# Kernel optimization log

Measured on AMD Instinct MI355X. Metric: run time of the kernel, lower is better.

## Reference

```python
import jax, jax.numpy as jnp
import numpy as np

HEADS = 16
GROUPS = 4
C_IN = 1024
C_OUT = 1024


def att_linear(x, w, b):
    # x: [B,S,C_in], w: [G, C_in/G, C_out/G], b: [C_out]
    B, S, _ = x.shape
    xg = x.reshape(B, S, GROUPS, C_IN // GROUPS)
    out = jnp.einsum('bsgi,gio->bsgo', xg, w).reshape(B, S, C_OUT)
    return out + b


def restricted_softmax(score, margin=0.0):
    # clamp row max at 0, add exp(margin - max) margin term to denominator
    smax = jnp.maximum(jnp.max(score, axis=-1, keepdims=True), 0.0)
    e = jnp.exp(score - smax)
    return e / (jnp.sum(e, axis=-1, keepdims=True) + jnp.exp(margin - smax))


def setup_inputs() -> dict:
    key = jax.random.key(0)
    ks = jax.random.split(key, 9)
    B, S = 4, 1024
    dpg_in, dpg_out = C_IN // GROUPS, C_OUT // GROUPS
    wscale = 1.0 / np.sqrt(dpg_in)
    return {
        'query': jax.random.normal(ks[0], (B, S, C_IN), jnp.float32),
        'key': jax.random.normal(ks[1], (B, S, C_IN), jnp.float32),
        'value': jax.random.normal(ks[2], (B, S, C_IN), jnp.float32),
        'wq': jax.random.uniform(ks[3], (GROUPS, dpg_in, dpg_out), jnp.float32, -wscale, wscale),
        'bq': jax.random.uniform(ks[4], (C_OUT,), jnp.float32, -wscale, wscale),
        'wk': jax.random.uniform(ks[5], (GROUPS, dpg_in, dpg_out), jnp.float32, -wscale, wscale),
        'bk': jax.random.uniform(ks[6], (C_OUT,), jnp.float32, -wscale, wscale),
        'wv': jax.random.uniform(ks[7], (GROUPS, dpg_in, dpg_out), jnp.float32, -wscale, wscale),
        'bv': jax.random.uniform(ks[8], (C_OUT,), jnp.float32, -wscale, wscale),
    }


def reference(query, key, value, wq, bq, wk, bk, wv, bv):
    B, S, _ = query.shape
    d = C_OUT // HEADS
    q = att_linear(query, wq, bq).reshape(B, S, HEADS, d).transpose(0, 2, 1, 3)
    k = att_linear(key, wk, bk).reshape(B, S, HEADS, d).transpose(0, 2, 1, 3)
    v = att_linear(value, wv, bv).reshape(B, S, HEADS, d).transpose(0, 2, 1, 3)
    score = jnp.einsum('bhqd,bhkd->bhqk', q, k) / jnp.sqrt(jnp.float32(d))
    attn = restricted_softmax(score)  # dropout p=0
    out = jnp.einsum('bhqk,bhkd->bhqd', attn, v)
    return out.transpose(0, 2, 1, 3).reshape(B, S, C_OUT)
```

## Files before the change

### kernel.cpp

```cpp
#include <hip/hip_runtime.h>
#include <hip/hip_bf16.h>

#define HEADS   16
#define GROUPS  4
#define C_IN    1024
#define C_OUT   1024
#define BATCH   4
#define SEQ     1024
#define DHEAD   64
#define DPG     256
#define MROWS   (BATCH * SEQ)
#define NBH     (BATCH * HEADS)
#define W_ELEMS ((size_t)GROUPS * DPG * DPG)
#define N_ELEMS ((size_t)NBH * SEQ * DHEAD)

typedef short  bhalf8  __attribute__((ext_vector_type(8)));
typedef short  short4v __attribute__((ext_vector_type(4)));
typedef float  f32x4   __attribute__((ext_vector_type(4)));
typedef unsigned short ushort8v __attribute__((ext_vector_type(8)));

#define MFMA16 __builtin_amdgcn_mfma_f32_16x16x32_bf16

__device__ __forceinline__ unsigned short f2bf(float x) {
    union { __hip_bfloat16 b; unsigned short u; } c;
    c.b = __float2bfloat16(x);
    return c.u;
}
__device__ __forceinline__ float bf2f(unsigned short s) {
    return __uint_as_float(((unsigned int)s) << 16);
}

__global__ void wsplit(const float* __restrict__ w0,
                       const float* __restrict__ w1,
                       const float* __restrict__ w2,
                       unsigned short* __restrict__ wtbase)
{
    const int tid = threadIdx.x;
    const int kt = blockIdx.x, ot = blockIdx.y;
    const int which = blockIdx.z >> 2, g = blockIdx.z & 3;
    const float* w = (which == 0) ? w0 : (which == 1) ? w1 : w2;
    unsigned short* wth = wtbase + (size_t)which * 2 * W_ELEMS;
    unsigned short* wtl = wth + W_ELEMS;

    __shared__ float Ls[64][68];
    const float* wg = w + (size_t)g * DPG * DPG;
#pragma unroll
    for (int p = 0; p < 4; ++p) {
        const int kk = 16 * p + (tid >> 4);
        const int oo = 4 * (tid & 15);
        const float4 v = *reinterpret_cast<const float4*>(
            wg + (size_t)(kt * 64 + kk) * DPG + ot * 64 + oo);
        Ls[kk][oo + 0] = v.x; Ls[kk][oo + 1] = v.y;
        Ls[kk][oo + 2] = v.z; Ls[kk][oo + 3] = v.w;
    }
    __syncthreads();
    unsigned short* th = wth + (size_t)g * DPG * DPG;
    unsigned short* tl = wtl + (size_t)g * DPG * DPG;
#pragma unroll
    for (int p = 0; p < 4; ++p) {
        const int oo = 16 * p + (tid >> 4);
        const int k4 = 4 * (tid & 15);
        ushort4 hv, lv;
        {
            float v0 = Ls[k4 + 0][oo], v1 = Ls[k4 + 1][oo];
            float v2 = Ls[k4 + 2][oo], v3 = Ls[k4 + 3][oo];
            hv.x = f2bf(v0); lv.x = f2bf(v0 - bf2f(hv.x));
            hv.y = f2bf(v1); lv.y = f2bf(v1 - bf2f(hv.y));
            hv.z = f2bf(v2); lv.z = f2bf(v2 - bf2f(hv.z));
            hv.w = f2bf(v3); lv.w = f2bf(v3 - bf2f(hv.w));
        }
        const size_t o = (size_t)(ot * 64 + oo) * DPG + kt * 64 + k4;
        *reinterpret_cast<ushort4*>(th + o) = hv;
        *reinterpret_cast<ushort4*>(tl + o) = lv;
    }
}

__launch_bounds__(256, 2)
__global__ void proj_mfma(const float* __restrict__ xq,
                          const float* __restrict__ xk,
                          const float* __restrict__ xv,
                          const unsigned short* __restrict__ wtbase,
                          const float* __restrict__ bq,
                          const float* __restrict__ bk,
                          const float* __restrict__ bv,
                          unsigned short* __restrict__ outbase)
{
    const int tid  = threadIdx.x;
    const int wave = tid >> 6;
    const int lane = tid & 63;
    const int h    = lane >> 4;
    const int ln   = lane & 15;
    const int mq   = wave >> 1;
    const int nq   = wave & 1;
    const int bx   = blockIdx.x;
    const int by   = blockIdx.y;
    const int which = blockIdx.z >> 2, g = blockIdx.z & 3;
    const int m0   = bx * 64;

    const float* x    = (which == 0) ? xq : (which == 1) ? xk : xv;
    const float* bias = (which == 0) ? bq : (which == 1) ? bk : bv;
    unsigned short* outh = outbase + (size_t)which * 2 * N_ELEMS;
    unsigned short* outl = outh + N_ELEMS;

    __shared__ uint4 smem4[3072];
    char* sp = (char*)smem4;

    f32x4 acc[2][4];
#pragma unroll
    for (int a = 0; a < 2; ++a)
#pragma unroll
        for (int b = 0; b < 4; ++b) acc[a][b] = (f32x4){0.f, 0.f, 0.f, 0.f};

    const float* xg = x + (size_t)m0 * C_IN + g * DPG;
    const unsigned short* wh = wtbase + (size_t)which * 2 * W_ELEMS
                             + ((size_t)g * DPG + by * 128) * DPG;
    const unsigned short* wl = wh + W_ELEMS;

    const int arb = tid >> 4, ac = tid & 15;
    const int brb = tid >> 3, bc = tid & 7;

    float4   ar[4];
    ushort8v brh[4], brl[4];
#pragma unroll
    for (int p = 0; p < 4; ++p)
        ar[p] = *reinterpret_cast<const float4*>(xg + (size_t)(16 * p + arb) * C_IN + 4 * ac);
#pragma unroll
    for (int p = 0; p < 4; ++p) {
        const size_t gofs = (size_t)(32 * p + brb) * DPG + 8 * bc;
        brh[p] = *reinterpret_cast<const ushort8v*>(wh + gofs);
        brl[p] = *reinterpret_cast<const ushort8v*>(wl + gofs);
    }

    for (int it = 0; it < 4; ++it) {
        if (it > 0) __syncthreads();
#pragma unroll
        for (int p = 0; p < 4; ++p) {
            const int rr = 16 * p + arb;
            const float4 v = ar[p];
            ushort4 hv, lv;
            hv.x = f2bf(v.x); lv.x = f2bf(v.x - bf2f(hv.x));
            hv.y = f2bf(v.y); lv.y = f2bf(v.y - bf2f(hv.y));
            hv.z = f2bf(v.z); lv.z = f2bf(v.z - bf2f(hv.z));
            hv.w = f2bf(v.w); lv.w = f2bf(v.w - bf2f(hv.w));
            const int off = (8 * ac) ^ ((rr & 7) << 4);
            *reinterpret_cast<ushort4*>(sp + rr * 128 + off) = hv;
            *reinterpret_cast<ushort4*>(sp + 8192 + rr * 128 + off) = lv;
        }
#pragma unroll
        for (int p = 0; p < 4; ++p) {
            const int rr = 32 * p + brb;
            const int off = (16 * bc) ^ ((rr & 7) << 4);
            *reinterpret_cast<ushort8v*>(sp + 16384 + rr * 128 + off) = brh[p];
            *reinterpret_cast<ushort8v*>(sp + 32768 + rr * 128 + off) = brl[p];
        }
        __syncthreads();

        if (it < 3) {
            const int k0n = (it + 1) * 64;
#pragma unroll
            for (int p = 0; p < 4; ++p)
                ar[p] = *reinterpret_cast<const float4*>(
                    xg + (size_t)(16 * p + arb) * C_IN + k0n + 4 * ac);
#pragma unroll
            for (int p = 0; p < 4; ++p) {
                const size_t gofs = (size_t)(32 * p + brb) * DPG + k0n + 8 * bc;
                brh[p] = *reinterpret_cast<const ushort8v*>(wh + gofs);
                brl[p] = *reinterpret_cast<const ushort8v*>(wl + gofs);
            }
        }

#pragma unroll
        for (int kk = 0; kk < 2; ++kk) {
            bhalf8 ah[2], al[2], bh_[4], bl_[4];
#pragma unroll
            for (int mt = 0; mt < 2; ++mt) {
                const int row = 32 * mq + 16 * mt + ln;
                const int off = (64 * kk + 16 * h) ^ ((row & 7) << 4);
                ah[mt] = *reinterpret_cast<const bhalf8*>(sp + row * 128 + off);
                al[mt] = *reinterpret_cast<const bhalf8*>(sp + 8192 + row * 128 + off);
            }
#pragma unroll
            for (int nt = 0; nt < 4; ++nt) {
                const int row = 64 * nq + 16 * nt + ln;
                const int off = (64 * kk + 16 * h) ^ ((row & 7) << 4);
                bh_[nt] = *reinterpret_cast<const bhalf8*>(sp + 16384 + row * 128 + off);
                bl_[nt] = *reinterpret_cast<const bhalf8*>(sp + 32768 + row * 128 + off);
            }
#pragma unroll
            for (int mt = 0; mt < 2; ++mt)
#pragma unroll
                for (int nt = 0; nt < 4; ++nt) {
                    acc[mt][nt] = MFMA16(ah[mt], bh_[nt], acc[mt][nt], 0, 0, 0);
                    acc[mt][nt] = MFMA16(al[mt], bh_[nt], acc[mt][nt], 0, 0, 0);
                    acc[mt][nt] = MFMA16(ah[mt], bl_[nt], acc[mt][nt], 0, 0, 0);
                }
        }
    }
    __syncthreads();

    const int hd = g * 4 + by * 2 + nq;
    const int b  = bx >> 4;
    const size_t bhb = ((size_t)b * HEADS + hd) * (SEQ * DHEAD);
    const int wbase = wave * 8192;
    const int sg0 = (bx & 15) * 64 + 32 * mq;
    const float oscale = (which == 0) ? 0.125f : 1.0f;
    float bnt[4];
#pragma unroll
    for (int nt = 0; nt < 4; ++nt)
        bnt[nt] = bias[g * 256 + by * 128 + 64 * nq + 16 * nt + ln];

    if (which != 2) {
#pragma unroll
        for (int mt = 0; mt < 2; ++mt)
#pragma unroll
            for (int nt = 0; nt < 4; ++nt)
#pragma unroll
                for (int r = 0; r < 4; ++r) {
                    const int sl = 16 * mt + 4 * h + r;
                    const float v = (acc[mt][nt][r] + bnt[nt]) * oscale;
                    const unsigned short hh = f2bf(v);
                    const unsigned short ll = f2bf(v - bf2f(hh));
                    const int cb = (2 * (16 * nt + ln)) ^ ((sl & 7) << 4);
                    *reinterpret_cast<unsigned short*>(sp + wbase + sl * 128 + cb) = hh;
                    *reinterpret_cast<unsigned short*>(sp + wbase + 4096 + sl * 128 + cb) = ll;
                }
        __syncthreads();
#pragma unroll
        for (int p = 0; p < 4; ++p) {
            const int sl = 8 * p + (lane >> 3);
            const int cb = (16 * (lane & 7)) ^ ((sl & 7) << 4);
            const size_t go = bhb + (size_t)(sg0 + sl) * 64 + 8 * (lane & 7);
            *reinterpret_cast<ushort8v*>(outh + go) =
                *reinterpret_cast<const ushort8v*>(sp + wbase + sl * 128 + cb);
            *reinterpret_cast<ushort8v*>(outl + go) =
                *reinterpret_cast<const ushort8v*>(sp + wbase + 4096 + sl * 128 + cb);
        }
    } else {
#pragma unroll
        for (int mt = 0; mt < 2; ++mt)
#pragma unroll
            for (int nt = 0; nt < 4; ++nt) {
                const int dl = 16 * nt + ln;
                ushort4 hv, lv;
                {
                    float v0 = acc[mt][nt][0] + bnt[nt];
                    float v1 = acc[mt][nt][1] + bnt[nt];
                    float v2 = acc[mt][nt][2] + bnt[nt];
                    float v3 = acc[mt][nt][3] + bnt[nt];
                    hv.x = f2bf(v0); lv.x = f2bf(v0 - bf2f(hv.x));
                    hv.y = f2bf(v1); lv.y = f2bf(v1 - bf2f(hv.y));
                    hv.z = f2bf(v2); lv.z = f2bf(v2 - bf2f(hv.z));
                    hv.w = f2bf(v3); lv.w = f2bf(v3 - bf2f(hv.w));
                }
                const int off = (32 * mt + 8 * h) ^ ((dl & 7) << 3);
                *reinterpret_cast<ushort4*>(sp + wbase + dl * 64 + off) = hv;
                *reinterpret_cast<ushort4*>(sp + wbase + 4096 + dl * 64 + off) = lv;
            }
        __syncthreads();
#pragma unroll
        for (int p = 0; p < 4; ++p) {
            const int dl  = 16 * p + (lane >> 2);
            const int c16 = 16 * (lane & 3);
            const int o0b = (c16) ^ ((dl & 7) << 3);
            const int o1b = (c16 + 8) ^ ((dl & 7) << 3);
            const size_t go = bhb + (size_t)dl * SEQ + sg0 + 8 * (lane & 3);
            *reinterpret_cast<ushort4*>(outh + go) =
                *reinterpret_cast<const ushort4*>(sp + wbase + dl * 64 + o0b);
            *reinterpret_cast<ushort4*>(outh + go + 4) =
                *reinterpret_cast<const ushort4*>(sp + wbase + dl * 64 + o1b);
            *reinterpret_cast<ushort4*>(outl + go) =
                *reinterpret_cast<const ushort4*>(sp + wbase + 4096 + dl * 64 + o0b);
            *reinterpret_cast<ushort4*>(outl + go + 4) =
                *reinterpret_cast<const ushort4*>(sp + wbase + 4096 + dl * 64 + o1b);
        }
    }
}

__launch_bounds__(256, 2)
__global__ void attn_mfma(const unsigned short* __restrict__ qh,
                          const unsigned short* __restrict__ ql,
                          const unsigned short* __restrict__ kh,
                          const unsigned short* __restrict__ kl,
                          const unsigned short* __restrict__ vth,
                          const unsigned short* __restrict__ vtl,
                          float* __restrict__ out)
{
    const int tid  = threadIdx.x;
    const int wave = tid >> 6;
    const int lane = tid & 63;
    const int h    = lane >> 4;
    const int ln   = lane & 15;
    const int bh   = blockIdx.x;
    const int q0   = blockIdx.y * 128 + wave * 32;

    const size_t bhbase = (size_t)bh * (SEQ * DHEAD);
    const unsigned short* qhp = qh + bhbase;
    const unsigned short* qlp = ql + bhbase;
    const unsigned short* khp = kh + bhbase;
    const unsigned short* klp = kl + bhbase;
    const unsigned short* vhp = vth + bhbase;
    const unsigned short* vlp = vtl + bhbase;

    __shared__ uint4 smem4[2048];
    char* sb = (char*)smem4;

    bhalf8 Qf[2][2][2];
#pragma unroll
    for (int nt = 0; nt < 2; ++nt)
#pragma unroll
        for (int dt = 0; dt < 2; ++dt) {
            const size_t o = (size_t)(q0 + 16 * nt + ln) * DHEAD + dt * 32 + 8 * h;
            Qf[nt][dt][0] = *reinterpret_cast<const bhalf8*>(qhp + o);
            Qf[nt][dt][1] = *reinterpret_cast<const bhalf8*>(qlp + o);
        }

    f32x4 accO[2][4];
#pragma unroll
    for (int a = 0; a < 2; ++a)
#pragma unroll
        for (int b = 0; b < 4; ++b) accO[a][b] = (f32x4){0.f, 0.f, 0.f, 0.f};
    float m_i[2] = {0.f, 0.f};
    float l_i[2] = {1.f, 1.f};

    const int r = tid >> 2, c = tid & 3;
    const int swz = (r & 7) << 4;
    const int d0 = r * 128 + ((c * 32) ^ swz);
    const int d1 = r * 128 + ((c * 32 + 16) ^ swz);
    const size_t gKr = (size_t)r * DHEAD + c * 16;
    const size_t gVr = (size_t)r * SEQ + c * 16;

    uint4 pr[8];
    {
        pr[0] = *reinterpret_cast<const uint4*>(khp + gKr);
        pr[1] = *reinterpret_cast<const uint4*>(khp + gKr + 8);
        pr[2] = *reinterpret_cast<const uint4*>(klp + gKr);
        pr[3] = *reinterpret_cast<const uint4*>(klp + gKr + 8);
        pr[4] = *reinterpret_cast<const uint4*>(vhp + gVr);
        pr[5] = *reinterpret_cast<const uint4*>(vhp + gVr + 8);
        pr[6] = *reinterpret_cast<const uint4*>(vlp + gVr);
        pr[7] = *reinterpret_cast<const uint4*>(vlp + gVr + 8);
    }

    for (int kt16 = 0; kt16 < 16; ++kt16) {
        if (kt16 > 0) __syncthreads();
        *reinterpret_cast<uint4*>(sb + d0)         = pr[0];
        *reinterpret_cast<uint4*>(sb + d1)         = pr[1];
        *reinterpret_cast<uint4*>(sb + 8192 + d0)  = pr[2];
        *reinterpret_cast<uint4*>(sb + 8192 + d1)  = pr[3];
        *reinterpret_cast<uint4*>(sb + 16384 + d0) = pr[4];
        *reinterpret_cast<uint4*>(sb + 16384 + d1) = pr[5];
        *reinterpret_cast<uint4*>(sb + 24576 + d0) = pr[6];
        *reinterpret_cast<uint4*>(sb + 24576 + d1) = pr[7];
        __syncthreads();

        if (kt16 < 15) {
            const size_t gK = gKr + (size_t)(kt16 + 1) * 64 * DHEAD;
            const size_t gV = gVr + (size_t)(kt16 + 1) * 64;
            pr[0] = *reinterpret_cast<const uint4*>(khp + gK);
            pr[1] = *reinterpret_cast<const uint4*>(khp + gK + 8);
            pr[2] = *reinterpret_cast<const uint4*>(klp + gK);
            pr[3] = *reinterpret_cast<const uint4*>(klp + gK + 8);
            pr[4] = *reinterpret_cast<const uint4*>(vhp + gV);
            pr[5] = *reinterpret_cast<const uint4*>(vhp + gV + 8);
            pr[6] = *reinterpret_cast<const uint4*>(vlp + gV);
            pr[7] = *reinterpret_cast<const uint4*>(vlp + gV + 8);
        }

        f32x4 s_[2][4];
#pragma unroll
        for (int a = 0; a < 2; ++a)
#pragma unroll
            for (int b = 0; b < 4; ++b) s_[a][b] = (f32x4){0.f, 0.f, 0.f, 0.f};
#pragma unroll
        for (int mt = 0; mt < 4; ++mt) {
            const int rr = 16 * mt + ln;
            const int sw = (rr & 7) << 4;
            const bhalf8 Ah0 = *reinterpret_cast<const bhalf8*>(sb + rr * 128 + ((16 * h) ^ sw));
            const bhalf8 Ah1 = *reinterpret_cast<const bhalf8*>(sb + rr * 128 + ((64 + 16 * h) ^ sw));
            const bhalf8 Al0 = *reinterpret_cast<const bhalf8*>(sb + 8192 + rr * 128 + ((16 * h) ^ sw));
            const bhalf8 Al1 = *reinterpret_cast<const bhalf8*>(sb + 8192 + rr * 128 + ((64 + 16 * h) ^ sw));
#pragma unroll
            for (int nt = 0; nt < 2; ++nt) {
                s_[nt][mt] = MFMA16(Ah0, Qf[nt][0][0], s_[nt][mt], 0, 0, 0);
                s_[nt][mt] = MFMA16(Ah1, Qf[nt][1][0], s_[nt][mt], 0, 0, 0);
                s_[nt][mt] = MFMA16(Ah0, Qf[nt][0][1], s_[nt][mt], 0, 0, 0);
                s_[nt][mt] = MFMA16(Ah1, Qf[nt][1][1], s_[nt][mt], 0, 0, 0);
                s_[nt][mt] = MFMA16(Al0, Qf[nt][0][0], s_[nt][mt], 0, 0, 0);
                s_[nt][mt] = MFMA16(Al1, Qf[nt][1][0], s_[nt][mt], 0, 0, 0);
            }
        }

        float Pv[2][4][4];
        bhalf8 Pfh[2][2], Pfl[2][2];
#pragma unroll
        for (int nt = 0; nt < 2; ++nt) {
            float mloc = -1e30f;
#pragma unroll
            for (int mt = 0; mt < 4; ++mt)
#pragma unroll
                for (int rr = 0; rr < 4; ++rr) {
                    const float v = s_[nt][mt][rr];
                    Pv[nt][mt][rr] = v;
                    mloc = fmaxf(mloc, v);
                }
            mloc = fmaxf(mloc, __shfl_xor(mloc, 16));
            mloc = fmaxf(mloc, __shfl_xor(mloc, 32));
            const float mn = fmaxf(m_i[nt], mloc);
            const float sf = __expf(m_i[nt] - mn);
            m_i[nt] = mn;
            float rs = 0.f;
#pragma unroll
            for (int mt = 0; mt < 4; ++mt)
#pragma unroll
                for (int rr = 0; rr < 4; ++rr) {
                    const float p = __expf(Pv[nt][mt][rr] - mn);
                    Pv[nt][mt][rr] = p;
                    rs += p;
                }
            rs += __shfl_xor(rs, 16);
            rs += __shfl_xor(rs, 32);
            l_i[nt] = l_i[nt] * sf + rs;
#pragma unroll
            for (int rr = 0; rr < 4; ++rr) {
                const float sf_b = __shfl(sf, 20 * h + rr);
#pragma unroll
                for (int ntd = 0; ntd < 4; ++ntd) accO[nt][ntd][rr] *= sf_b;
            }
#pragma unroll
            for (int kt = 0; kt < 2; ++kt) {
                bhalf8 fh, fl;
#pragma unroll
                for (int j = 0; j < 8; ++j) {
                    const float p = Pv[nt][2 * kt + (j >> 2)][j & 3];
                    const unsigned short hi = f2bf(p);
                    fh[j] = (short)hi;
                    fl[j] = (short)f2bf(p - bf2f(hi));
                }
                Pfh[nt][kt] = fh;
                Pfl[nt][kt] = fl;
            }
        }

#pragma unroll
        for (int kt = 0; kt < 2; ++kt) {
#pragma unroll
            for (int ntd = 0; ntd < 4; ++ntd) {
                const int rr = 16 * ntd + ln;
                const int sw = (rr & 7) << 4;
                const int c0 = (64 * kt + 8 * h) ^ sw;
                const int c1 = (64 * kt + 32 + 8 * h) ^ sw;
                union { short4v q[2]; bhalf8 v; } ubh, ubl;
                ubh.q[0] = *reinterpret_cast<const short4v*>(sb + 16384 + rr * 128 + c0);
                ubh.q[1] = *reinterpret_cast<const short4v*>(sb + 16384 + rr * 128 + c1);
                ubl.q[0] = *reinterpret_cast<const short4v*>(sb + 24576 + rr * 128 + c0);
                ubl.q[1] = *reinterpret_cast<const short4v*>(sb + 24576 + rr * 128 + c1);
                const bhalf8 Bh = ubh.v;
                const bhalf8 Bl = ubl.v;
#pragma unroll
                for (int nt = 0; nt < 2; ++nt) {
                    accO[nt][ntd] = MFMA16(Pfh[nt][kt], Bh, accO[nt][ntd], 0, 0, 0);
                    accO[nt][ntd] = MFMA16(Pfh[nt][kt], Bl, accO[nt][ntd], 0, 0, 0);
                    accO[nt][ntd] = MFMA16(Pfl[nt][kt], Bh, accO[nt][ntd], 0, 0, 0);
                }
            }
        }
    }

    const int bB = bh >> 4;
    const int hd = bh & 15;
#pragma unroll
    for (int nt = 0; nt < 2; ++nt) {
        float linv[4];
#pragma unroll
        for (int rr = 0; rr < 4; ++rr) linv[rr] = 1.0f / __shfl(l_i[nt], 20 * h + rr);
#pragma unroll
        for (int rr = 0; rr < 4; ++rr) {
            const int q = q0 + 16 * nt + 4 * h + rr;
            float* orow = out + ((size_t)bB * SEQ + q) * C_OUT + hd * DHEAD + ln;
#pragma unroll
            for (int ntd = 0; ntd < 4; ++ntd)
                orow[16 * ntd] = accO[nt][ntd][rr] * linv[rr];
        }
    }
}

extern "C" void kernel_launch(void* const* d_in, const int* in_sizes, int n_in,
                              void* d_out, int out_size, void* d_ws, size_t ws_size,
                              hipStream_t stream) {
    const float* query = (const float*)d_in[0];
    const float* key   = (const float*)d_in[1];
    const float* value = (const float*)d_in[2];
    const float* wq    = (const float*)d_in[3];
    const float* bq    = (const float*)d_in[4];
    const float* wk    = (const float*)d_in[5];
    const float* bk    = (const float*)d_in[6];
    const float* wv    = (const float*)d_in[7];
    const float* bv    = (const float*)d_in[8];

    unsigned short* qkv = (unsigned short*)d_ws;
    unsigned short* wts = qkv + 6 * N_ELEMS;

    dim3 blk(256);
    wsplit<<<dim3(4, 4, 12), blk, 0, stream>>>(wq, wk, wv, wts);
    proj_mfma<<<dim3(MROWS / 64, 2, 12), blk, 0, stream>>>(
        query, key, value, wts, bq, bk, bv, qkv);

    attn_mfma<<<dim3(NBH, SEQ / 128), blk, 0, stream>>>(
        qkv, qkv + N_ELEMS, qkv + 2 * N_ELEMS, qkv + 3 * N_ELEMS,
        qkv + 4 * N_ELEMS, qkv + 5 * N_ELEMS, (float*)d_out);
}
```

Measured before the change: 224.5 us.

## Stage K/V and weight tiles via direct global-to-LDS loads with double buffering

```diff
diff --git a/kernel.cpp b/kernel.cpp
--- a/kernel.cpp
+++ b/kernel.cpp
@@ -28,6 +28,13 @@
 }
 __device__ __forceinline__ float bf2f(unsigned short s) {
     return __uint_as_float(((unsigned int)s) << 16);
+}
+
+__device__ __forceinline__ void gload16(const void* gsrc, void* lds) {
+    __builtin_amdgcn_global_load_lds(
+        (const __attribute__((address_space(1))) unsigned int*)(unsigned long long)(uintptr_t)gsrc,
+        (__attribute__((address_space(3))) unsigned int*)(unsigned int)(uintptr_t)lds,
+        16, 0, 0);
 }
 
 __global__ void wsplit(const float* __restrict__ w0,
@@ -116,27 +123,31 @@
                              + ((size_t)g * DPG + by * 128) * DPG;
     const unsigned short* wl = wh + W_ELEMS;
 
+    int b_goff[4], b_lds[4];
+#pragma unroll
+    for (int c = 0; c < 4; ++c) {
+        const int o  = (c * 4 + wave) * 1024 + lane * 16;
+        const int rw = o >> 7;
+        const int kidx = ((o & 127) ^ ((rw & 7) << 4)) >> 1;
+        b_goff[c] = rw * DPG + kidx;
+        b_lds[c]  = (c * 4 + wave) * 1024;
+    }
+
     const int arb = tid >> 4, ac = tid & 15;
-    const int brb = tid >> 3, bc = tid & 7;
-
-    float4   ar[4];
-    ushort8v brh[4], brl[4];
-#pragma unroll
-    for (int p = 0; p < 4; ++p)
-        ar[p] = *reinterpret_cast<const float4*>(xg + (size_t)(16 * p + arb) * C_IN + 4 * ac);
-#pragma unroll
-    for (int p = 0; p < 4; ++p) {
-        const size_t gofs = (size_t)(32 * p + brb) * DPG + 8 * bc;
-        brh[p] = *reinterpret_cast<const ushort8v*>(wh + gofs);
-        brl[p] = *reinterpret_cast<const ushort8v*>(wl + gofs);
-    }
 
     for (int it = 0; it < 4; ++it) {
+        const int k0 = it * 64;
         if (it > 0) __syncthreads();
+#pragma unroll
+        for (int c = 0; c < 4; ++c) {
+            gload16(wh + b_goff[c] + k0, sp + 16384 + b_lds[c]);
+            gload16(wl + b_goff[c] + k0, sp + 32768 + b_lds[c]);
+        }
 #pragma unroll
         for (int p = 0; p < 4; ++p) {
             const int rr = 16 * p + arb;
-            const float4 v = ar[p];
+            const float4 v = *reinterpret_cast<const float4*>(
+                xg + (size_t)rr * C_IN + k0 + 4 * ac);
             ushort4 hv, lv;
             hv.x = f2bf(v.x); lv.x = f2bf(v.x - bf2f(hv.x));
             hv.y = f2bf(v.y); lv.y = f2bf(v.y - bf2f(hv.y));
@@ -146,28 +157,7 @@
             *reinterpret_cast<ushort4*>(sp + rr * 128 + off) = hv;
             *reinterpret_cast<ushort4*>(sp + 8192 + rr * 128 + off) = lv;
         }
-#pragma unroll
-        for (int p = 0; p < 4; ++p) {
-            const int rr = 32 * p + brb;
-            const int off = (16 * bc) ^ ((rr & 7) << 4);
-            *reinterpret_cast<ushort8v*>(sp + 16384 + rr * 128 + off) = brh[p];
-            *reinterpret_cast<ushort8v*>(sp + 32768 + rr * 128 + off) = brl[p];
-        }
         __syncthreads();
-
-        if (it < 3) {
-            const int k0n = (it + 1) * 64;
-#pragma unroll
-            for (int p = 0; p < 4; ++p)
-                ar[p] = *reinterpret_cast<const float4*>(
-                    xg + (size_t)(16 * p + arb) * C_IN + k0n + 4 * ac);
-#pragma unroll
-            for (int p = 0; p < 4; ++p) {
-                const size_t gofs = (size_t)(32 * p + brb) * DPG + k0n + 8 * bc;
-                brh[p] = *reinterpret_cast<const ushort8v*>(wh + gofs);
-                brl[p] = *reinterpret_cast<const ushort8v*>(wl + gofs);
-            }
-        }
 
 #pragma unroll
         for (int kk = 0; kk < 2; ++kk) {
@@ -301,7 +291,7 @@
     const unsigned short* vhp = vth + bhbase;
     const unsigned short* vlp = vtl + bhbase;
 
-    __shared__ uint4 smem4[2048];
+    __shared__ uint4 smem4[4096];
     char* sb = (char*)smem4;
 
     bhalf8 Qf[2][2][2];
@@ -322,49 +312,37 @@
     float m_i[2] = {0.f, 0.f};
     float l_i[2] = {1.f, 1.f};
 
-    const int r = tid >> 2, c = tid & 3;
-    const int swz = (r & 7) << 4;
-    const int d0 = r * 128 + ((c * 32) ^ swz);
-    const int d1 = r * 128 + ((c * 32 + 16) ^ swz);
-    const size_t gKr = (size_t)r * DHEAD + c * 16;
-    const size_t gVr = (size_t)r * SEQ + c * 16;
-
-    uint4 pr[8];
-    {
-        pr[0] = *reinterpret_cast<const uint4*>(khp + gKr);
-        pr[1] = *reinterpret_cast<const uint4*>(khp + gKr + 8);
-        pr[2] = *reinterpret_cast<const uint4*>(klp + gKr);
-        pr[3] = *reinterpret_cast<const uint4*>(klp + gKr + 8);
-        pr[4] = *reinterpret_cast<const uint4*>(vhp + gVr);
-        pr[5] = *reinterpret_cast<const uint4*>(vhp + gVr + 8);
-        pr[6] = *reinterpret_cast<const uint4*>(vlp + gVr);
-        pr[7] = *reinterpret_cast<const uint4*>(vlp + gVr + 8);
-    }
-
-    for (int kt16 = 0; kt16 < 16; ++kt16) {
-        if (kt16 > 0) __syncthreads();
-        *reinterpret_cast<uint4*>(sb + d0)         = pr[0];
-        *reinterpret_cast<uint4*>(sb + d1)         = pr[1];
-        *reinterpret_cast<uint4*>(sb + 8192 + d0)  = pr[2];
-        *reinterpret_cast<uint4*>(sb + 8192 + d1)  = pr[3];
-        *reinterpret_cast<uint4*>(sb + 16384 + d0) = pr[4];
-        *reinterpret_cast<uint4*>(sb + 16384 + d1) = pr[5];
-        *reinterpret_cast<uint4*>(sb + 24576 + d0) = pr[6];
-        *reinterpret_cast<uint4*>(sb + 24576 + d1) = pr[7];
-        __syncthreads();
-
-        if (kt16 < 15) {
-            const size_t gK = gKr + (size_t)(kt16 + 1) * 64 * DHEAD;
-            const size_t gV = gVr + (size_t)(kt16 + 1) * 64;
-            pr[0] = *reinterpret_cast<const uint4*>(khp + gK);
-            pr[1] = *reinterpret_cast<const uint4*>(khp + gK + 8);
-            pr[2] = *reinterpret_cast<const uint4*>(klp + gK);
-            pr[3] = *reinterpret_cast<const uint4*>(klp + gK + 8);
-            pr[4] = *reinterpret_cast<const uint4*>(vhp + gV);
-            pr[5] = *reinterpret_cast<const uint4*>(vhp + gV + 8);
-            pr[6] = *reinterpret_cast<const uint4*>(vlp + gV);
-            pr[7] = *reinterpret_cast<const uint4*>(vlp + gV + 8);
-        }
+    int rw_[2], kd_[2], lofs_[2];
+#pragma unroll
+    for (int c = 0; c < 2; ++c) {
+        const int o = (c * 4 + wave) * 1024 + lane * 16;
+        rw_[c]   = o >> 7;
+        kd_[c]   = ((o & 127) ^ ((rw_[c] & 7) << 4)) >> 1;
+        lofs_[c] = (c * 4 + wave) * 1024;
+    }
+
+#define STAGE_TILE(BUF, K0)                                                        \
+    do {                                                                           \
+        _Pragma("unroll")                                                          \
+        for (int c = 0; c < 2; ++c) {                                              \
+            char* lb = sb + (BUF) + lofs_[c];                                      \
+            const int rw = rw_[c], kd = kd_[c];                                    \
+            gload16(khp + (size_t)((K0) + rw) * DHEAD + kd, lb);                   \
+            gload16(klp + (size_t)((K0) + rw) * DHEAD + kd, lb + 8192);            \
+            gload16(vhp + (size_t)rw * SEQ + (K0) + kd,     lb + 16384);           \
+            gload16(vlp + (size_t)rw * SEQ + (K0) + kd,     lb + 24576);           \
+        }                                                                          \
+    } while (0)
+
+    STAGE_TILE(0, 0);
+
+    for (int t = 0; t < 16; ++t) {
+        const int nb = ((t + 1) & 1) * 32768;
+        const int nk = ((t + 1) & 15) * 64;
+        STAGE_TILE(nb, nk);
+        asm volatile("s_waitcnt vmcnt(8)\n\ts_barrier" ::: "memory");
+
+        const char* cb = sb + (t & 1) * 32768;
 
         f32x4 s_[2][4];
 #pragma unroll
@@ -375,10 +353,10 @@
         for (int mt = 0; mt < 4; ++mt) {
             const int rr = 16 * mt + ln;
             const int sw = (rr & 7) << 4;
-            const bhalf8 Ah0 = *reinterpret_cast<const bhalf8*>(sb + rr * 128 + ((16 * h) ^ sw));
-            const bhalf8 Ah1 = *reinterpret_cast<const bhalf8*>(sb + rr * 128 + ((64 + 16 * h) ^ sw));
-            const bhalf8 Al0 = *reinterpret_cast<const bhalf8*>(sb + 8192 + rr * 128 + ((16 * h) ^ sw));
-            const bhalf8 Al1 = *reinterpret_cast<const bhalf8*>(sb + 8192 + rr * 128 + ((64 + 16 * h) ^ sw));
+            const bhalf8 Ah0 = *reinterpret_cast<const bhalf8*>(cb + rr * 128 + ((16 * h) ^ sw));
+            const bhalf8 Ah1 = *reinterpret_cast<const bhalf8*>(cb + rr * 128 + ((64 + 16 * h) ^ sw));
+            const bhalf8 Al0 = *reinterpret_cast<const bhalf8*>(cb + 8192 + rr * 128 + ((16 * h) ^ sw));
+            const bhalf8 Al1 = *reinterpret_cast<const bhalf8*>(cb + 8192 + rr * 128 + ((64 + 16 * h) ^ sw));
 #pragma unroll
             for (int nt = 0; nt < 2; ++nt) {
                 s_[nt][mt] = MFMA16(Ah0, Qf[nt][0][0], s_[nt][mt], 0, 0, 0);
@@ -450,10 +428,10 @@
                 const int c0 = (64 * kt + 8 * h) ^ sw;
                 const int c1 = (64 * kt + 32 + 8 * h) ^ sw;
                 union { short4v q[2]; bhalf8 v; } ubh, ubl;
-                ubh.q[0] = *reinterpret_cast<const short4v*>(sb + 16384 + rr * 128 + c0);
-                ubh.q[1] = *reinterpret_cast<const short4v*>(sb + 16384 + rr * 128 + c1);
-                ubl.q[0] = *reinterpret_cast<const short4v*>(sb + 24576 + rr * 128 + c0);
-                ubl.q[1] = *reinterpret_cast<const short4v*>(sb + 24576 + rr * 128 + c1);
+                ubh.q[0] = *reinterpret_cast<const short4v*>(cb + 16384 + rr * 128 + c0);
+                ubh.q[1] = *reinterpret_cast<const short4v*>(cb + 16384 + rr * 128 + c1);
+                ubl.q[0] = *reinterpret_cast<const short4v*>(cb + 24576 + rr * 128 + c0);
+                ubl.q[1] = *reinterpret_cast<const short4v*>(cb + 24576 + rr * 128 + c1);
                 const bhalf8 Bh = ubh.v;
                 const bhalf8 Bl = ubl.v;
 #pragma unroll
@@ -464,7 +442,9 @@
                 }
             }
         }
-    }
+        asm volatile("s_barrier" ::: "memory");
+    }
+    asm volatile("s_waitcnt vmcnt(0)" ::: "memory");
 
     const int bB = bh >> 4;
     const int hd = bh & 15;
@@ -482,6 +462,7 @@
                 orow[16 * ntd] = accO[nt][ntd][rr] * linv[rr];
         }
     }
+#undef STAGE_TILE
 }
 
 extern "C" void kernel_launch(void* const* d_in, const int* in_sizes, int n_in,
```

Result: faster. 191.7 us (-14.6%).
